# Kernel tuning notes

Hardware: AMD Instinct MI355X
Metric: run time of the kernel (lower is better)

## Reference

```python
import jax, jax.numpy as jnp
import numpy as np


def _cdist(p1, p2):
    # Euclidean cdist via the matmul expansion (matches torch.cdist p=2 fast path):
    # ||a-b||^2 = ||a||^2 + ||b||^2 - 2 a.b ; clamp tiny negatives before sqrt.
    sq1 = jnp.sum(p1 * p1, axis=-1, keepdims=True)        # (N, 1)
    sq2 = jnp.sum(p2 * p2, axis=-1, keepdims=True).T      # (1, M)
    d2 = sq1 + sq2 - 2.0 * (p1 @ p2.T)                    # (N, M)
    return jnp.sqrt(jnp.maximum(d2, 0.0))


def setup_inputs() -> dict:
    key = jax.random.key(0)
    k1, k2 = jax.random.split(key)
    N, M = 16384, 16384
    points1 = jax.random.normal(k1, (N, 3), dtype=jnp.float32)
    points2 = jax.random.normal(k2, (M, 3), dtype=jnp.float32)
    return {"points1": points1, "points2": points2}


def reference(points1, points2):
    dist = _cdist(points1, points2)                        # (N, M)
    min1 = jnp.min(dist, axis=1)                           # (N,) nearest in points2
    min2 = jnp.min(dist, axis=0)                           # (M,) nearest in points1
    return jnp.sum(min1) + jnp.sum(min2)
```

## Files before the change

kernel.cpp:

```cpp
#include <hip/hip_runtime.h>
#include <hip/hip_bf16.h>
#include <math.h>


typedef _Float16 half8    __attribute__((ext_vector_type(8)));
typedef float    floatx16 __attribute__((ext_vector_type(16)));

constexpr int CH    = 2048;
constexpr int RT    = 2;
constexpr int WROWS = RT * 32;
constexpr int ROWS  = 4 * WROWS;
constexpr int BLK   = 256;

__global__ __launch_bounds__(BLK, 4) void chamfer_sweep_kernel(
    const float* __restrict__ P1, const float* __restrict__ P2,
    float* __restrict__ part, int n1, int n2, int YC)
{
    __shared__ uint2 sB[CH];
    __shared__ float sRowMin[ROWS];

    const int dir  = blockIdx.z;
    const float* A = dir == 0 ? P1 : P2;
    const float* B = dir == 0 ? P2 : P1;
    const int nA   = dir == 0 ? n1 : n2;
    const int nB   = dir == 0 ? n2 : n1;
    float* pbase   = part + (dir == 0 ? 0 : (size_t)YC * n1);

    const int tid  = threadIdx.x;
    const int wave = tid >> 6;
    const int lane = tid & 63;
    const int n    = lane & 31;
    const int g    = lane >> 5;
    const bool g0  = (g == 0);

    const int bstart = blockIdx.y * CH;
    for (int i = tid; i < CH; i += BLK) {
        int j = bstart + i; if (j >= nB) j = nB - 1;
        float bx = B[3*j], by = B[3*j+1], bz = B[3*j+2];
        _Float16 hx = (_Float16)bx, hy = (_Float16)by, hz = (_Float16)bz;
        float qx = (float)hx, qy = (float)hy, qz = (float)hz;
        _Float16 hw = (_Float16)(qx*qx + qy*qy + qz*qz);
        union { _Float16 h[4]; uint2 u; } p;
        p.h[0] = hx; p.h[1] = hy; p.h[2] = hz; p.h[3] = hw;
        sB[i] = p.u;
    }

    const _Float16 h0 = (_Float16)0.0f;
    half8 af[RT];
#pragma unroll
    for (int t = 0; t < RT; ++t) {
        int row = blockIdx.x * ROWS + wave * WROWS + t * 32 + n;
        if (row >= nA) row = nA - 1;
        float ax = A[3*row], ay = A[3*row+1], az = A[3*row+2];
        _Float16 hax = (_Float16)ax, hay = (_Float16)ay, haz = (_Float16)az;
        float qx = (float)hax, qy = (float)hay, qz = (float)haz;
        _Float16 hs = (_Float16)(qx*qx + qy*qy + qz*qz);
        af[t][0] = g0 ? (_Float16)(-2.0f * qx) : h0;
        af[t][1] = g0 ? (_Float16)(-2.0f * qy) : h0;
        af[t][2] = g0 ? (_Float16)(-2.0f * qz) : h0;
        af[t][3] = g0 ? (_Float16)1.0f : h0;
        af[t][4] = g0 ? hs : h0;
        af[t][5] = h0; af[t][6] = h0; af[t][7] = h0;
    }
    unsigned c2;
    { union { _Float16 h[2]; unsigned u; } q;
      q.h[0] = (_Float16)1.0f; q.h[1] = h0; c2 = q.u; }

    __syncthreads();

    floatx16 rowmin[RT];
#pragma unroll
    for (int t = 0; t < RT; ++t)
#pragma unroll
        for (int r = 0; r < 16; ++r) rowmin[t][r] = 1e30f;
    const floatx16 zacc = {};

#pragma unroll 2
    for (int bt = 0; bt < CH / 64; ++bt) {
        uint2 b0 = sB[bt * 64 + n];
        uint2 b1 = sB[bt * 64 + 32 + n];
        union { half8 v; unsigned u[4]; } bu0, bu1;
        bu0.u[0] = b0.x; bu0.u[1] = b0.y; bu0.u[2] = c2; bu0.u[3] = 0u;
        bu1.u[0] = b1.x; bu1.u[1] = b1.y; bu1.u[2] = c2; bu1.u[3] = 0u;

        floatx16 d00 = __builtin_amdgcn_mfma_f32_32x32x16_f16(af[0], bu0.v, zacc, 0, 0, 0);
        floatx16 d01 = __builtin_amdgcn_mfma_f32_32x32x16_f16(af[0], bu1.v, zacc, 0, 0, 0);
        floatx16 d10 = __builtin_amdgcn_mfma_f32_32x32x16_f16(af[1], bu0.v, zacc, 0, 0, 0);
        floatx16 d11 = __builtin_amdgcn_mfma_f32_32x32x16_f16(af[1], bu1.v, zacc, 0, 0, 0);

#pragma unroll
        for (int r = 0; r < 16; ++r) {
            rowmin[0][r] = fminf(fminf(rowmin[0][r], d00[r]), d01[r]);
            rowmin[1][r] = fminf(fminf(rowmin[1][r], d10[r]), d11[r]);
        }
    }

#pragma unroll
    for (int mask = 1; mask <= 16; mask <<= 1) {
#pragma unroll
        for (int t = 0; t < RT; ++t)
#pragma unroll
            for (int r = 0; r < 16; ++r)
                rowmin[t][r] = fminf(rowmin[t][r], __shfl_xor(rowmin[t][r], mask));
    }
    if (n == 0) {
#pragma unroll
        for (int t = 0; t < RT; ++t)
#pragma unroll
            for (int r = 0; r < 16; ++r) {
                int rr = wave * WROWS + t * 32 + g * 4 + ((r & 3) + 8 * (r >> 2));
                sRowMin[rr] = rowmin[t][r];
            }
    }
    __syncthreads();

    {
        int grow = blockIdx.x * ROWS + tid;
        if (grow < nA) pbase[(size_t)blockIdx.y * nA + grow] = sRowMin[tid];
    }
}

__global__ __launch_bounds__(256) void reduce1_kernel(
    const float* __restrict__ part, float* __restrict__ bsum,
    int n1, int n2, int YC)
{
    __shared__ float s[256];
    int r = blockIdx.x * 256 + threadIdx.x;
    float acc = 0.0f;
    int ntot = n1 + n2;
    if (r < ntot) {
        const float* p; int row, nA;
        if (r < n1) { p = part;                       row = r;      nA = n1; }
        else        { p = part + (size_t)YC * n1;     row = r - n1; nA = n2; }
        float m = 1e30f;
        for (int y = 0; y < YC; ++y) m = fminf(m, p[(size_t)y * nA + row]);
        acc = sqrtf(fmaxf(m, 0.0f));
    }
    s[threadIdx.x] = acc;
    __syncthreads();
    for (int w = 128; w > 0; w >>= 1) {
        if (threadIdx.x < w) s[threadIdx.x] += s[threadIdx.x + w];
        __syncthreads();
    }
    if (threadIdx.x == 0) bsum[blockIdx.x] = s[0];
}

__global__ __launch_bounds__(256) void reduce2_kernel(
    const float* __restrict__ bsum, int nb, float* __restrict__ out)
{
    __shared__ float s[256];
    float acc = 0.0f;
    for (int i = threadIdx.x; i < nb; i += 256) acc += bsum[i];
    s[threadIdx.x] = acc;
    __syncthreads();
    for (int w = 128; w > 0; w >>= 1) {
        if (threadIdx.x < w) s[threadIdx.x] += s[threadIdx.x + w];
        __syncthreads();
    }
    if (threadIdx.x == 0) out[0] = s[0];
}

extern "C" void kernel_launch(void* const* d_in, const int* in_sizes, int n_in,
                              void* d_out, int out_size, void* d_ws, size_t ws_size,
                              hipStream_t stream) {
    const float* P1 = (const float*)d_in[0];
    const float* P2 = (const float*)d_in[1];
    const int n1 = in_sizes[0] / 3;
    const int n2 = in_sizes[1] / 3;
    const int nmax = (n1 > n2) ? n1 : n2;
    const int YC = (nmax + CH - 1) / CH;

    float* part = (float*)d_ws;
    float* bsum = part + (size_t)YC * (n1 + n2);
    float* out  = (float*)d_out;

    {
        dim3 grid((nmax + ROWS - 1) / ROWS, YC, 2);
        chamfer_sweep_kernel<<<grid, BLK, 0, stream>>>(P1, P2, part, n1, n2, YC);
    }
    int nb = (n1 + n2 + 255) / 256;
    reduce1_kernel<<<nb, 256, 0, stream>>>(part, bsum, n1, n2, YC);
    reduce2_kernel<<<1, 256, 0, stream>>>(bsum, nb, out);
}
```

Measured before the change: 83.11 us.

## Pad B to 16-byte LDS entries, prefetch next tile, transpose partial-min layout

Each B point is now stored in LDS as a full 16-byte half8 (constant 1 and zeros baked in), so the MFMA operand comes from a single vector load with no per-iteration register assembly. The next iteration's B operands are software-prefetched into registers. The partial-min buffer becomes row-major over Y chunks, which changes the reduce kernel's access pattern. The occupancy hint in launch bounds is dropped. Costs are doubled LDS for sB (32KB), which may reduce blocks per CU, and strided global writes from the sweep kernel.

```diff
diff --git a/kernel.cpp b/kernel.cpp
--- a/kernel.cpp
+++ b/kernel.cpp
@@ -12,11 +12,11 @@
 constexpr int ROWS  = 4 * WROWS;
 constexpr int BLK   = 256;
 
-__global__ __launch_bounds__(BLK, 4) void chamfer_sweep_kernel(
+__global__ __launch_bounds__(BLK) void chamfer_sweep_kernel(
     const float* __restrict__ P1, const float* __restrict__ P2,
     float* __restrict__ part, int n1, int n2, int YC)
 {
-    __shared__ uint2 sB[CH];
+    __shared__ uint4 sB[CH];
     __shared__ float sRowMin[ROWS];
 
     const int dir  = blockIdx.z;
@@ -40,8 +40,10 @@
         _Float16 hx = (_Float16)bx, hy = (_Float16)by, hz = (_Float16)bz;
         float qx = (float)hx, qy = (float)hy, qz = (float)hz;
         _Float16 hw = (_Float16)(qx*qx + qy*qy + qz*qz);
-        union { _Float16 h[4]; uint2 u; } p;
+        union { _Float16 h[8]; uint4 u; } p;
         p.h[0] = hx; p.h[1] = hy; p.h[2] = hz; p.h[3] = hw;
+        p.h[4] = (_Float16)1.0f; p.h[5] = (_Float16)0.0f;
+        p.h[6] = (_Float16)0.0f; p.h[7] = (_Float16)0.0f;
         sB[i] = p.u;
     }
 
@@ -62,9 +64,6 @@
         af[t][4] = g0 ? hs : h0;
         af[t][5] = h0; af[t][6] = h0; af[t][7] = h0;
     }
-    unsigned c2;
-    { union { _Float16 h[2]; unsigned u; } q;
-      q.h[0] = (_Float16)1.0f; q.h[1] = h0; c2 = q.u; }
 
     __syncthreads();
 
@@ -75,18 +74,22 @@
         for (int r = 0; r < 16; ++r) rowmin[t][r] = 1e30f;
     const floatx16 zacc = {};
 
+    constexpr int ITERS = CH / 64;
+    const uint4* bp = sB + n;
+    uint4 q0 = bp[0];
+    uint4 q1 = bp[32];
 #pragma unroll 2
-    for (int bt = 0; bt < CH / 64; ++bt) {
-        uint2 b0 = sB[bt * 64 + n];
-        uint2 b1 = sB[bt * 64 + 32 + n];
-        union { half8 v; unsigned u[4]; } bu0, bu1;
-        bu0.u[0] = b0.x; bu0.u[1] = b0.y; bu0.u[2] = c2; bu0.u[3] = 0u;
-        bu1.u[0] = b1.x; bu1.u[1] = b1.y; bu1.u[2] = c2; bu1.u[3] = 0u;
+    for (int bt = 0; bt < ITERS; ++bt) {
+        union { uint4 u; half8 v; } b0, b1;
+        b0.u = q0; b1.u = q1;
+        int nx = (bt + 1) & (ITERS - 1);
+        q0 = bp[nx * 64];
+        q1 = bp[nx * 64 + 32];
 
-        floatx16 d00 = __builtin_amdgcn_mfma_f32_32x32x16_f16(af[0], bu0.v, zacc, 0, 0, 0);
-        floatx16 d01 = __builtin_amdgcn_mfma_f32_32x32x16_f16(af[0], bu1.v, zacc, 0, 0, 0);
-        floatx16 d10 = __builtin_amdgcn_mfma_f32_32x32x16_f16(af[1], bu0.v, zacc, 0, 0, 0);
-        floatx16 d11 = __builtin_amdgcn_mfma_f32_32x32x16_f16(af[1], bu1.v, zacc, 0, 0, 0);
+        floatx16 d00 = __builtin_amdgcn_mfma_f32_32x32x16_f16(af[0], b0.v, zacc, 0, 0, 0);
+        floatx16 d01 = __builtin_amdgcn_mfma_f32_32x32x16_f16(af[0], b1.v, zacc, 0, 0, 0);
+        floatx16 d10 = __builtin_amdgcn_mfma_f32_32x32x16_f16(af[1], b0.v, zacc, 0, 0, 0);
+        floatx16 d11 = __builtin_amdgcn_mfma_f32_32x32x16_f16(af[1], b1.v, zacc, 0, 0, 0);
 
 #pragma unroll
         for (int r = 0; r < 16; ++r) {
@@ -116,7 +119,7 @@
 
     {
         int grow = blockIdx.x * ROWS + tid;
-        if (grow < nA) pbase[(size_t)blockIdx.y * nA + grow] = sRowMin[tid];
+        if (grow < nA) pbase[(size_t)grow * YC + blockIdx.y] = sRowMin[tid];
     }
 }
 
@@ -129,11 +132,9 @@
     float acc = 0.0f;
     int ntot = n1 + n2;
     if (r < ntot) {
-        const float* p; int row, nA;
-        if (r < n1) { p = part;                       row = r;      nA = n1; }
-        else        { p = part + (size_t)YC * n1;     row = r - n1; nA = n2; }
+        const float* p = part + (size_t)r * YC;
         float m = 1e30f;
-        for (int y = 0; y < YC; ++y) m = fminf(m, p[(size_t)y * nA + row]);
+        for (int y = 0; y < YC; ++y) m = fminf(m, p[y]);
         acc = sqrtf(fmaxf(m, 0.0f));
     }
     s[threadIdx.x] = acc;
```

Result: slower. 89.57 us (+7.8%).

## Drop per-wave row tiling to one 32-row tile and transpose partial-min layout

Applied to the files above, without the earlier changes.

Each wave now handles a single 32-row A tile instead of two, halving block rows to 128 and doubling the grid in x. The B-sweep loop is unrolled 4 instead of 2. Each B chunk is now reused by half as many rows, so total LDS staging work and B loads from global memory double. In exchange the kernel uses fewer registers and exposes more parallelism. The partial-min buffer switches to row-major [row][YC], so the reduce kernel reads contiguous YC values per row, but the sweep kernel's stores become strided.

```diff
diff --git a/kernel.cpp b/kernel.cpp
--- a/kernel.cpp
+++ b/kernel.cpp
@@ -6,11 +6,9 @@
 typedef _Float16 half8    __attribute__((ext_vector_type(8)));
 typedef float    floatx16 __attribute__((ext_vector_type(16)));
 
-constexpr int CH    = 2048;
-constexpr int RT    = 2;
-constexpr int WROWS = RT * 32;
-constexpr int ROWS  = 4 * WROWS;
-constexpr int BLK   = 256;
+constexpr int CH   = 2048;
+constexpr int ROWS = 128;
+constexpr int BLK  = 256;
 
 __global__ __launch_bounds__(BLK, 4) void chamfer_sweep_kernel(
     const float* __restrict__ P1, const float* __restrict__ P2,
@@ -46,21 +44,20 @@
     }
 
     const _Float16 h0 = (_Float16)0.0f;
-    half8 af[RT];
-#pragma unroll
-    for (int t = 0; t < RT; ++t) {
-        int row = blockIdx.x * ROWS + wave * WROWS + t * 32 + n;
+    half8 af;
+    {
+        int row = blockIdx.x * ROWS + wave * 32 + n;
         if (row >= nA) row = nA - 1;
         float ax = A[3*row], ay = A[3*row+1], az = A[3*row+2];
         _Float16 hax = (_Float16)ax, hay = (_Float16)ay, haz = (_Float16)az;
         float qx = (float)hax, qy = (float)hay, qz = (float)haz;
         _Float16 hs = (_Float16)(qx*qx + qy*qy + qz*qz);
-        af[t][0] = g0 ? (_Float16)(-2.0f * qx) : h0;
-        af[t][1] = g0 ? (_Float16)(-2.0f * qy) : h0;
-        af[t][2] = g0 ? (_Float16)(-2.0f * qz) : h0;
-        af[t][3] = g0 ? (_Float16)1.0f : h0;
-        af[t][4] = g0 ? hs : h0;
-        af[t][5] = h0; af[t][6] = h0; af[t][7] = h0;
+        af[0] = g0 ? (_Float16)(-2.0f * qx) : h0;
+        af[1] = g0 ? (_Float16)(-2.0f * qy) : h0;
+        af[2] = g0 ? (_Float16)(-2.0f * qz) : h0;
+        af[3] = g0 ? (_Float16)1.0f : h0;
+        af[4] = g0 ? hs : h0;
+        af[5] = h0; af[6] = h0; af[7] = h0;
     }
     unsigned c2;
     { union { _Float16 h[2]; unsigned u; } q;
@@ -68,14 +65,12 @@
 
     __syncthreads();
 
-    floatx16 rowmin[RT];
+    floatx16 rowmin;
 #pragma unroll
-    for (int t = 0; t < RT; ++t)
-#pragma unroll
-        for (int r = 0; r < 16; ++r) rowmin[t][r] = 1e30f;
+    for (int r = 0; r < 16; ++r) rowmin[r] = 1e30f;
     const floatx16 zacc = {};
 
-#pragma unroll 2
+#pragma unroll 4
     for (int bt = 0; bt < CH / 64; ++bt) {
         uint2 b0 = sB[bt * 64 + n];
         uint2 b1 = sB[bt * 64 + 32 + n];
@@ -83,40 +78,32 @@
         bu0.u[0] = b0.x; bu0.u[1] = b0.y; bu0.u[2] = c2; bu0.u[3] = 0u;
         bu1.u[0] = b1.x; bu1.u[1] = b1.y; bu1.u[2] = c2; bu1.u[3] = 0u;
 
-        floatx16 d00 = __builtin_amdgcn_mfma_f32_32x32x16_f16(af[0], bu0.v, zacc, 0, 0, 0);
-        floatx16 d01 = __builtin_amdgcn_mfma_f32_32x32x16_f16(af[0], bu1.v, zacc, 0, 0, 0);
-        floatx16 d10 = __builtin_amdgcn_mfma_f32_32x32x16_f16(af[1], bu0.v, zacc, 0, 0, 0);
-        floatx16 d11 = __builtin_amdgcn_mfma_f32_32x32x16_f16(af[1], bu1.v, zacc, 0, 0, 0);
+        floatx16 d0 = __builtin_amdgcn_mfma_f32_32x32x16_f16(af, bu0.v, zacc, 0, 0, 0);
+        floatx16 d1 = __builtin_amdgcn_mfma_f32_32x32x16_f16(af, bu1.v, zacc, 0, 0, 0);
 
 #pragma unroll
-        for (int r = 0; r < 16; ++r) {
-            rowmin[0][r] = fminf(fminf(rowmin[0][r], d00[r]), d01[r]);
-            rowmin[1][r] = fminf(fminf(rowmin[1][r], d10[r]), d11[r]);
-        }
+        for (int r = 0; r < 16; ++r)
+            rowmin[r] = fminf(fminf(rowmin[r], d0[r]), d1[r]);
     }
 
 #pragma unroll
-    for (int mask = 1; mask <= 16; mask <<= 1) {
+    for (int mask = 1; mask <= 16; mask <<= 1)
 #pragma unroll
-        for (int t = 0; t < RT; ++t)
-#pragma unroll
-            for (int r = 0; r < 16; ++r)
-                rowmin[t][r] = fminf(rowmin[t][r], __shfl_xor(rowmin[t][r], mask));
-    }
+        for (int r = 0; r < 16; ++r)
+            rowmin[r] = fminf(rowmin[r], __shfl_xor(rowmin[r], mask));
+
     if (n == 0) {
 #pragma unroll
-        for (int t = 0; t < RT; ++t)
-#pragma unroll
-            for (int r = 0; r < 16; ++r) {
-                int rr = wave * WROWS + t * 32 + g * 4 + ((r & 3) + 8 * (r >> 2));
-                sRowMin[rr] = rowmin[t][r];
-            }
+        for (int r = 0; r < 16; ++r) {
+            int rr = wave * 32 + g * 4 + ((r & 3) + 8 * (r >> 2));
+            sRowMin[rr] = rowmin[r];
+        }
     }
     __syncthreads();
 
-    {
+    if (tid < ROWS) {
         int grow = blockIdx.x * ROWS + tid;
-        if (grow < nA) pbase[(size_t)blockIdx.y * nA + grow] = sRowMin[tid];
+        if (grow < nA) pbase[(size_t)grow * YC + blockIdx.y] = sRowMin[tid];
     }
 }
 
@@ -129,11 +116,9 @@
     float acc = 0.0f;
     int ntot = n1 + n2;
     if (r < ntot) {
-        const float* p; int row, nA;
-        if (r < n1) { p = part;                       row = r;      nA = n1; }
-        else        { p = part + (size_t)YC * n1;     row = r - n1; nA = n2; }
+        const float* p = part + (size_t)r * YC;
         float m = 1e30f;
-        for (int y = 0; y < YC; ++y) m = fminf(m, p[(size_t)y * nA + row]);
+        for (int y = 0; y < YC; ++y) m = fminf(m, p[y]);
         acc = sqrtf(fmaxf(m, 0.0f));
     }
     s[threadIdx.x] = acc;
```

New measurement: 80.68 us. 2.9% less time.
